# Optimization experiments

Measured on AMD Instinct MI355X. Metric: run time of the kernel, lower is better.

Reference implementation:

```python
import jax, jax.numpy as jnp
import numpy as np

B, S, CACHE, HID, NH, NKV, HD, INTER = 2, 1024, 2048, 2048, 8, 1, 256, 16384
EPS = 1e-6
SOFTCAP = 50.0
SCALE = HD ** -0.5  # query_pre_attn_scalar is None -> head_dim**-0.5
NEG = -1e9


def _rms(x, w, eps=EPS):
    # Gemma RMSNorm: fp32 norm, output scaled by (1 + weight)
    x32 = x.astype(jnp.float32)
    n = x32 * jax.lax.rsqrt(jnp.mean(x32 * x32, axis=-1, keepdims=True) + eps)
    return (n * (1.0 + w)).astype(x.dtype)


def _rope(x, cos, sin):
    # half-split complex rotation (Gemma apply_rotary_emb): first half real, second half imag
    d2 = x.shape[-1] // 2
    x1, x2 = x[..., :d2], x[..., d2:]
    c = cos[None, :, None, :]
    s = sin[None, :, None, :]
    return jnp.concatenate([x1 * c - x2 * s, x1 * s + x2 * c], axis=-1).astype(x.dtype)


def setup_inputs() -> dict:
    key = jax.random.key(0)
    ks = jax.random.split(key, 8)
    sc = lambda k, sh, f: jax.random.normal(k, sh, jnp.float32) * f
    inp = {}
    inp["hidden_states"] = sc(ks[0], (B, S, HID), 1.0)
    inv = 1.0 / (10000.0 ** (np.arange(0, HD, 2, dtype=np.float32) / HD))
    t = np.arange(S, dtype=np.float32)[:, None] * inv[None, :]
    inp["cos"] = jnp.asarray(np.cos(t), jnp.float32)
    inp["sin"] = jnp.asarray(np.sin(t), jnp.float32)
    inp["kv_write_indices"] = jnp.arange(S, dtype=jnp.int32)
    inp["k_cache"] = jnp.zeros((B, CACHE, NKV, HD), jnp.float32)
    inp["v_cache"] = jnp.zeros((B, CACHE, NKV, HD), jnp.float32)
    i = jnp.arange(S)[:, None]
    j = jnp.arange(CACHE)[None, :]
    inp["mask"] = jnp.where(j <= i, 0.0, NEG).astype(jnp.float32)[None, None]  # [1,1,S,CACHE]
    inp["w_qkv"] = sc(ks[1], ((NH + 2 * NKV) * HD, HID), 0.02)
    inp["w_o"] = sc(ks[2], (HID, NH * HD), 0.02)
    inp["w_gate"] = sc(ks[3], (INTER, HID), 0.02)
    inp["w_up"] = sc(ks[4], (INTER, HID), 0.02)
    inp["w_down"] = sc(ks[5], (HID, INTER), 0.02)
    inp["ln_in"] = jnp.zeros((HID,), jnp.float32)
    inp["ln_post"] = jnp.zeros((HID,), jnp.float32)
    inp["q_norm"] = jnp.zeros((HD,), jnp.float32)
    inp["k_norm"] = jnp.zeros((HD,), jnp.float32)
    return inp


def reference(hidden_states, cos, sin, kv_write_indices, k_cache, v_cache, mask,
              w_qkv, w_o, w_gate, w_up, w_down, ln_in, ln_post, q_norm, k_norm):
    # ---- attention sub-block ----
    res = hidden_states
    x = _rms(hidden_states, ln_in)
    qkv = x @ w_qkv.T  # [B,S,(NH+2*NKV)*HD]
    xq, xk, xv = jnp.split(qkv, [NH * HD, NH * HD + NKV * HD], axis=-1)
    xq = xq.reshape(B, S, NH, HD)
    xk = xk.reshape(B, S, NKV, HD)
    xv = xv.reshape(B, S, NKV, HD)
    xq = _rms(xq, q_norm)  # QK-norm
    xk = _rms(xk, k_norm)
    xq = _rope(xq, cos, sin)
    xk = _rope(xk, cos, sin)
    # KV-cache write (index_copy_ on dim 1)
    k_cache = k_cache.at[:, kv_write_indices].set(xk)
    v_cache = v_cache.at[:, kv_write_indices].set(xv)
    key = jnp.repeat(k_cache, NH // NKV, axis=2)  # [B,CACHE,NH,HD]
    val = jnp.repeat(v_cache, NH // NKV, axis=2)
    scores = jnp.einsum('bshd,bthd->bhst', xq * SCALE, key)  # [B,NH,S,CACHE]
    scores = jnp.tanh(scores / SOFTCAP) * SOFTCAP            # logit softcapping
    probs = jax.nn.softmax(scores + mask, axis=-1)
    out = jnp.einsum('bhst,bthd->bshd', probs, val).reshape(B, S, NH * HD)
    h = res + out @ w_o.T
    # ---- MLP sub-block ----
    res = h
    x = _rms(h, ln_post)
    gate = jax.nn.gelu(x @ w_gate.T, approximate=True)
    up = x @ w_up.T
    return res + (gate * up) @ w_down.T
```

## Files before the change

### kernel.cpp

```cpp
#include <hip/hip_runtime.h>
#include <hip/hip_bf16.h>

typedef __attribute__((ext_vector_type(8))) short short8;
typedef __attribute__((ext_vector_type(4))) float f32x4;
typedef unsigned short u16;

#define B_N 2
#define S_N 1024
#define HID_N 2048
#define NH_N 8
#define HD_N 256
#define INTER_N 16384

#define GLB(p) ((const __attribute__((address_space(1))) void*)(p))
#define AS3(p) ((__attribute__((address_space(3))) void*)(p))

__device__ inline u16 f2b_rn(float f) {
    union { float f; unsigned int u; } x; x.f = f;
    unsigned int r = x.u + 0x7fffu + ((x.u >> 16) & 1u);
    return (u16)(r >> 16);
}
__device__ inline float b2f(u16 h) {
    union { unsigned int u; float f; } x; x.u = ((unsigned int)h) << 16;
    return x.f;
}
__device__ inline float gelu_tanh(float x) {
    float x3 = x * x * x;
    return 0.5f * x * (1.f + tanhf(0.7978845608028654f * (x + 0.044715f * x3)));
}

__global__ __launch_bounds__(256) void convert_f2b(const float* __restrict__ in,
                                                   u16* __restrict__ out, int n4) {
    int i = blockIdx.x * 256 + threadIdx.x;
    int stride = gridDim.x * 256;
    for (; i < n4; i += stride) {
        float4 v = reinterpret_cast<const float4*>(in)[i];
        u16 o[4] = { f2b_rn(v.x), f2b_rn(v.y), f2b_rn(v.z), f2b_rn(v.w) };
        reinterpret_cast<ulonglong1*>(out)[i] = *reinterpret_cast<ulonglong1*>(o);
    }
}

__global__ __launch_bounds__(256) void rmsnorm_k(const float* __restrict__ x,
                                                 const float* __restrict__ w,
                                                 u16* __restrict__ out) {
    const int row = blockIdx.x;
    const int tid = threadIdx.x;
    const float* xr = x + (size_t)row * HID_N;
    const float4* xr4 = reinterpret_cast<const float4*>(xr);
    float4 a = xr4[tid * 2], b = xr4[tid * 2 + 1];
    float s = a.x*a.x + a.y*a.y + a.z*a.z + a.w*a.w
            + b.x*b.x + b.y*b.y + b.z*b.z + b.w*b.w;
    for (int off = 32; off > 0; off >>= 1) s += __shfl_xor(s, off, 64);
    __shared__ float red[4];
    if ((tid & 63) == 0) red[tid >> 6] = s;
    __syncthreads();
    float tot = red[0] + red[1] + red[2] + red[3];
    float inv = rsqrtf(tot * (1.0f / HID_N) + 1e-6f);
    const float4* w4 = reinterpret_cast<const float4*>(w);
    float4 wa = w4[tid * 2], wb = w4[tid * 2 + 1];
    short8 o;
    o[0] = (short)f2b_rn(a.x * inv * (1.f + wa.x));
    o[1] = (short)f2b_rn(a.y * inv * (1.f + wa.y));
    o[2] = (short)f2b_rn(a.z * inv * (1.f + wa.z));
    o[3] = (short)f2b_rn(a.w * inv * (1.f + wa.w));
    o[4] = (short)f2b_rn(b.x * inv * (1.f + wb.x));
    o[5] = (short)f2b_rn(b.y * inv * (1.f + wb.y));
    o[6] = (short)f2b_rn(b.z * inv * (1.f + wb.z));
    o[7] = (short)f2b_rn(b.w * inv * (1.f + wb.w));
    reinterpret_cast<short8*>(out + (size_t)row * HID_N)[tid] = o;
}

__global__ __launch_bounds__(256) void qkv_post_k(const float* __restrict__ qkv,
                                                  const float* __restrict__ cosb,
                                                  const float* __restrict__ sinb,
                                                  const int* __restrict__ kvw,
                                                  const float* __restrict__ qn,
                                                  const float* __restrict__ kn,
                                                  u16* __restrict__ qb,
                                                  u16* __restrict__ kb,
                                                  u16* __restrict__ vt) {
    const int bs = blockIdx.x;
    const int b = bs >> 10, s = bs & 1023;
    const int tid = threadIdx.x;
    const float* row = qkv + (size_t)bs * 2560;
    __shared__ float buf[256];
    __shared__ float red[4];
    const int sdst = kvw[s];
    const float cv = cosb[s * 128 + (tid & 127)];
    const float sv = sinb[s * 128 + (tid & 127)];
    for (int vi = 0; vi < 9; ++vi) {
        float val = row[vi * 256 + tid];
        float ss = val * val;
        for (int off = 32; off > 0; off >>= 1) ss += __shfl_xor(ss, off, 64);
        __syncthreads();
        if ((tid & 63) == 0) red[tid >> 6] = ss;
        __syncthreads();
        float ms = (red[0] + red[1] + red[2] + red[3]) * (1.f / 256.f) + 1e-6f;
        const float* nw = (vi < 8) ? qn : kn;
        float nrm = val * rsqrtf(ms) * (1.f + nw[tid]);
        buf[tid] = nrm;
        __syncthreads();
        float o;
        if (tid < 128) o = buf[tid] * cv - buf[tid + 128] * sv;
        else           o = buf[tid - 128] * sv + buf[tid] * cv;
        if (vi < 8) {
            qb[(((size_t)(b * 8 + vi)) * 1024 + s) * 256 + tid] = f2b_rn(o * 0.0625f);
        } else {
            kb[((size_t)(b * 1024 + sdst)) * 256 + tid] = f2b_rn(o);
        }
    }
    float vv = row[2304 + tid];
    vt[((size_t)(b * 256 + tid)) * 1024 + sdst] = f2b_rn(vv);
}

__global__ __launch_bounds__(256) void attn_k(const u16* __restrict__ qb,
                                              const u16* __restrict__ kb,
                                              const u16* __restrict__ vt,
                                              u16* __restrict__ out) {
    const int qt = blockIdx.x;
    const int h  = blockIdx.y;
    const int b  = blockIdx.z;
    const int tid = threadIdx.x, lane = tid & 63, wid = tid >> 6;
    const int g = lane >> 4, li = lane & 15;
    const int q0 = qt * 64 + wid * 16;
    __shared__ u16 pbuf[4][16 * 32];

    short8 qf[8];
    const size_t qbase = (((size_t)(b * 8 + h)) * 1024 + q0 + li) * 256;
    #pragma unroll
    for (int kk = 0; kk < 8; ++kk)
        qf[kk] = *reinterpret_cast<const short8*>(qb + qbase + kk * 32 + g * 8);

    f32x4 o[16];
    #pragma unroll
    for (int d = 0; d < 16; ++d) o[d] = f32x4{0.f, 0.f, 0.f, 0.f};
    float lsum[4] = {0.f, 0.f, 0.f, 0.f};

    const int nt = (qt * 64 + 64) / 32;
    for (int t = 0; t < nt; ++t) {
        const int kv0 = t * 32;
        f32x4 sc[2];
        sc[0] = f32x4{0.f, 0.f, 0.f, 0.f};
        sc[1] = f32x4{0.f, 0.f, 0.f, 0.f};
        #pragma unroll
        for (int ch = 0; ch < 2; ++ch) {
            const size_t kbase = ((size_t)(b * 1024 + kv0 + ch * 16 + li)) * 256;
            #pragma unroll
            for (int kk = 0; kk < 8; ++kk) {
                short8 kf = *reinterpret_cast<const short8*>(kb + kbase + kk * 32 + g * 8);
                sc[ch] = __builtin_amdgcn_mfma_f32_16x16x32_bf16(qf[kk], kf, sc[ch], 0, 0, 0);
            }
        }
        float pv[2][4];
        #pragma unroll
        for (int reg = 0; reg < 4; ++reg) {
            int qrow = q0 + g * 4 + reg;
            float rs = 0.f;
            #pragma unroll
            for (int ch = 0; ch < 2; ++ch) {
                int col = kv0 + ch * 16 + li;
                float s = sc[ch][reg];
                s = tanhf(s * 0.02f) * 50.f;
                float p = (col <= qrow) ? exp2f(s * 1.44269504f) : 0.f;
                pv[ch][reg] = p;
                rs += p;
            }
            for (int off = 1; off < 16; off <<= 1) rs += __shfl_xor(rs, off, 64);
            lsum[reg] += rs;
        }
        __syncthreads();
        #pragma unroll
        for (int reg = 0; reg < 4; ++reg)
            #pragma unroll
            for (int ch = 0; ch < 2; ++ch)
                pbuf[wid][(g * 4 + reg) * 32 + ch * 16 + li] = f2b_rn(pv[ch][reg]);
        __syncthreads();
        short8 pf = *reinterpret_cast<const short8*>(&pbuf[wid][li * 32 + g * 8]);
        #pragma unroll
        for (int dt = 0; dt < 16; ++dt) {
            const size_t vbase = ((size_t)(b * 256 + dt * 16 + li)) * 1024 + kv0 + g * 8;
            short8 vf = *reinterpret_cast<const short8*>(vt + vbase);
            o[dt] = __builtin_amdgcn_mfma_f32_16x16x32_bf16(pf, vf, o[dt], 0, 0, 0);
        }
    }
    #pragma unroll
    for (int reg = 0; reg < 4; ++reg) {
        int row = q0 + g * 4 + reg;
        float inv = 1.f / lsum[reg];
        #pragma unroll
        for (int dt = 0; dt < 16; ++dt) {
            out[((size_t)(b * 1024 + row)) * 2048 + h * 256 + dt * 16 + li] =
                f2b_rn(o[dt][reg] * inv);
        }
    }
}

template <int EPI>
__global__ __launch_bounds__(256) void gemm_bt(const u16* __restrict__ A,
                                               const u16* __restrict__ W,
                                               const float* __restrict__ res,
                                               float* __restrict__ outf,
                                               int M, int N, int K) {
    __shared__ u16 As[2][128 * 64];
    __shared__ u16 Bs[2][128 * 64];
    const int tid = threadIdx.x, lane = tid & 63, wid = tid >> 6;
    const int g = lane >> 4, li = lane & 15;
    const int wr = wid >> 1, wc = wid & 1;
    const int m0 = blockIdx.x * 128, n0 = blockIdx.y * 128;

    f32x4 acc[4][4];
    #pragma unroll
    for (int m = 0; m < 4; ++m)
        #pragma unroll
        for (int n = 0; n < 4; ++n) acc[m][n] = f32x4{0.f, 0.f, 0.f, 0.f};

    const int lrow = lane >> 3;
    const int lcol = (lane & 7) ^ lrow;
    const u16* ga0 = A + (size_t)(m0 + wid * 32 + lrow) * K + lcol * 8;
    const u16* gb0 = W + (size_t)(n0 + wid * 32 + lrow) * K + lcol * 8;
    const int lbase = wid * 32 * 64;

    auto STAGE = [&](int buf, int k0) {
        #pragma unroll
        for (int i = 0; i < 4; ++i) {
            __builtin_amdgcn_global_load_lds(GLB(ga0 + k0 + (size_t)(i * 8) * K),
                                             AS3(&As[buf][lbase + i * 8 * 64]), 16, 0, 0);
            __builtin_amdgcn_global_load_lds(GLB(gb0 + k0 + (size_t)(i * 8) * K),
                                             AS3(&Bs[buf][lbase + i * 8 * 64]), 16, 0, 0);
        }
    };

    const int NT = K >> 6;
    STAGE(0, 0);
    int cur = 0;
    for (int t = 0; t < NT; ++t) {
        if (t + 1 < NT) {
            STAGE(cur ^ 1, (t + 1) << 6);
            asm volatile("s_waitcnt vmcnt(8)" ::: "memory");
        } else {
            asm volatile("s_waitcnt vmcnt(0)" ::: "memory");
        }
        __builtin_amdgcn_s_barrier();
        __builtin_amdgcn_sched_barrier(0);
        #pragma unroll
        for (int kh = 0; kh < 2; ++kh) {
            short8 af[4], bfr[4];
            #pragma unroll
            for (int m = 0; m < 4; ++m) {
                int rw = wr * 64 + m * 16 + li;
                int slot = (kh * 4 + g) ^ (rw & 7);
                af[m] = *reinterpret_cast<const short8*>(&As[cur][rw * 64 + slot * 8]);
            }
            #pragma unroll
            for (int n = 0; n < 4; ++n) {
                int rw = wc * 64 + n * 16 + li;
                int slot = (kh * 4 + g) ^ (rw & 7);
                bfr[n] = *reinterpret_cast<const short8*>(&Bs[cur][rw * 64 + slot * 8]);
            }
            #pragma unroll
            for (int m = 0; m < 4; ++m)
                #pragma unroll
                for (int n = 0; n < 4; ++n)
                    acc[m][n] = __builtin_amdgcn_mfma_f32_16x16x32_bf16(af[m], bfr[n], acc[m][n], 0, 0, 0);
        }
        __builtin_amdgcn_sched_barrier(0);
        __builtin_amdgcn_s_barrier();
        cur ^= 1;
    }

    #pragma unroll
    for (int m = 0; m < 4; ++m) {
        #pragma unroll
        for (int n = 0; n < 4; ++n) {
            #pragma unroll
            for (int reg = 0; reg < 4; ++reg) {
                int row = m0 + wr * 64 + m * 16 + g * 4 + reg;
                int col = n0 + wc * 64 + n * 16 + li;
                size_t idx = (size_t)row * N + col;
                float v = acc[m][n][reg];
                if (EPI == 0) outf[idx] = v;
                else          outf[idx] = v + res[idx];
            }
        }
    }
}

template <int EPI>
__global__ __launch_bounds__(512, 2) void gemm256(const u16* __restrict__ A,
                                                  const u16* __restrict__ W,
                                                  const u16* __restrict__ gin,
                                                  float* __restrict__ outf,
                                                  u16* __restrict__ outb,
                                                  int M, int N, int K, int kcN) {
    __shared__ u16 As_[2][256 * 64];
    __shared__ u16 Bs_[2][256 * 64];
    const int tid = threadIdx.x, lane = tid & 63, wid = tid >> 6;
    const int g = lane >> 4, li = lane & 15;
    const int wm = wid >> 2, wn = wid & 3;
    const int m0 = blockIdx.x * 256, n0 = blockIdx.y * 256;

    int koff = 0, Keff = K;
    if (EPI == 4) {
        Keff = K / kcN;
        koff = blockIdx.z * Keff;
        outf += (size_t)blockIdx.z * M * N;
    }

    f32x4 acc[8][4];
    #pragma unroll
    for (int m = 0; m < 8; ++m)
        #pragma unroll
        for (int n = 0; n < 4; ++n) acc[m][n] = f32x4{0.f, 0.f, 0.f, 0.f};

    const int trow = tid >> 3;
    const int sgr = (tid & 7) ^ (trow & 7);
    const u16* gaS = A + (size_t)(m0 + trow) * K + koff + sgr * 8;
    const u16* gbS = W + (size_t)(n0 + trow) * K + koff + sgr * 8;
    const int ldst = (wid << 9);

    auto STAGE = [&](int buf, int k0) {
        #pragma unroll
        for (int i = 0; i < 4; ++i)
            __builtin_amdgcn_global_load_lds(GLB(gaS + k0 + (size_t)(i * 64) * K),
                                             AS3(&As_[buf][(i << 12) + ldst]), 16, 0, 0);
        #pragma unroll
        for (int i = 0; i < 4; ++i)
            __builtin_amdgcn_global_load_lds(GLB(gbS + k0 + (size_t)(i * 64) * K),
                                             AS3(&Bs_[buf][(i << 12) + ldst]), 16, 0, 0);
    };

    const int NT = Keff >> 6;
    STAGE(0, 0);
    int cur = 0;
    for (int t = 0; t < NT; ++t) {
        if (t + 1 < NT) {
            STAGE(cur ^ 1, (t + 1) << 6);
            asm volatile("s_waitcnt vmcnt(8)" ::: "memory");
        } else {
            asm volatile("s_waitcnt vmcnt(0)" ::: "memory");
        }
        __builtin_amdgcn_s_barrier();
        __builtin_amdgcn_sched_barrier(0);
        #pragma unroll
        for (int kh = 0; kh < 2; ++kh) {
            short8 af[8], bfr[4];
            #pragma unroll
            for (int m = 0; m < 8; ++m) {
                int rw = wm * 128 + m * 16 + li;
                int slot = (kh * 4 + g) ^ (rw & 7);
                af[m] = *reinterpret_cast<const short8*>(&As_[cur][rw * 64 + slot * 8]);
            }
            #pragma unroll
            for (int n = 0; n < 4; ++n) {
                int rw = wn * 64 + n * 16 + li;
                int slot = (kh * 4 + g) ^ (rw & 7);
                bfr[n] = *reinterpret_cast<const short8*>(&Bs_[cur][rw * 64 + slot * 8]);
            }
            #pragma unroll
            for (int m = 0; m < 8; ++m)
                #pragma unroll
                for (int n = 0; n < 4; ++n)
                    acc[m][n] = __builtin_amdgcn_mfma_f32_16x16x32_bf16(af[m], bfr[n], acc[m][n], 0, 0, 0);
        }
        __builtin_amdgcn_sched_barrier(0);
        __builtin_amdgcn_s_barrier();
        cur ^= 1;
    }

    #pragma unroll
    for (int m = 0; m < 8; ++m) {
        #pragma unroll
        for (int n = 0; n < 4; ++n) {
            #pragma unroll
            for (int reg = 0; reg < 4; ++reg) {
                int row = m0 + wm * 128 + m * 16 + g * 4 + reg;
                int col = n0 + wn * 64 + n * 16 + li;
                size_t idx = (size_t)row * N + col;
                float v = acc[m][n][reg];
                if (EPI == 2)      outb[idx] = f2b_rn(gelu_tanh(v));
                else if (EPI == 3) outb[idx] = f2b_rn(v * b2f(gin[idx]));
                else               outf[idx] = v;
            }
        }
    }
}

__global__ __launch_bounds__(256) void reduce4_k(const float* __restrict__ part,
                                                 const float* __restrict__ res,
                                                 float* __restrict__ out, int n4) {
    int i = blockIdx.x * 256 + threadIdx.x;
    int stride = gridDim.x * 256;
    const size_t ps = (size_t)HID_N * B_N * S_N / 4;
    const float4* p4 = reinterpret_cast<const float4*>(part);
    const float4* r4 = reinterpret_cast<const float4*>(res);
    float4* o4 = reinterpret_cast<float4*>(out);
    for (; i < n4; i += stride) {
        float4 a = p4[i], b = p4[i + ps], c = p4[i + 2 * ps], d = p4[i + 3 * ps];
        float4 r = r4[i];
        float4 o;
        o.x = r.x + a.x + b.x + c.x + d.x;
        o.y = r.y + a.y + b.y + c.y + d.y;
        o.z = r.z + a.z + b.z + c.z + d.z;
        o.w = r.w + a.w + b.w + c.w + d.w;
        o4[i] = o;
    }
}

extern "C" void kernel_launch(void* const* d_in, const int* in_sizes, int n_in,
                              void* d_out, int out_size, void* d_ws, size_t ws_size,
                              hipStream_t stream) {
    (void)in_sizes; (void)n_in; (void)out_size; (void)ws_size;
    const float* hs     = (const float*)d_in[0];
    const float* cosb   = (const float*)d_in[1];
    const float* sinb   = (const float*)d_in[2];
    const int*   kvw    = (const int*)d_in[3];
    const float* wqkv   = (const float*)d_in[7];
    const float* wo     = (const float*)d_in[8];
    const float* wg     = (const float*)d_in[9];
    const float* wu     = (const float*)d_in[10];
    const float* wd     = (const float*)d_in[11];
    const float* ln_in  = (const float*)d_in[12];
    const float* ln_post= (const float*)d_in[13];
    const float* qn     = (const float*)d_in[14];
    const float* kn     = (const float*)d_in[15];
    float* out = (float*)d_out;

    char* p = (char*)d_ws;
    auto alloc = [&](size_t bytes) {
        char* r = p;
        p += (bytes + 255) & ~(size_t)255;
        return r;
    };
    u16* wqkv_b = (u16*)alloc(2560ull * 2048 * 2);
    u16* wo_b   = (u16*)alloc(2048ull * 2048 * 2);
    u16* wg_b   = (u16*)alloc(16384ull * 2048 * 2);
    u16* wu_b   = (u16*)alloc(16384ull * 2048 * 2);
    u16* wd_b   = (u16*)alloc(2048ull * 16384 * 2);
    u16* xn     = (u16*)alloc(2048ull * 2048 * 2);
    float* qkvf = (float*)alloc(2048ull * 2560 * 4);
    u16* qbuf   = (u16*)alloc(2ull * 8 * 1024 * 256 * 2);
    u16* kbuf   = (u16*)alloc(2ull * 1024 * 256 * 2);
    u16* vtbuf  = (u16*)alloc(2ull * 256 * 1024 * 2);
    u16* attn_o = (u16*)alloc(2048ull * 2048 * 2);
    float* hbuf = (float*)alloc(2048ull * 2048 * 4);
    u16* x2     = (u16*)alloc(2048ull * 2048 * 2);
    u16* actb   = (u16*)alloc(2048ull * 16384 * 2);
    float* partials = (float*)d_ws;

    auto conv = [&](const float* src, u16* dst, long n) {
        int n4 = (int)(n / 4);
        long blk = (n4 + 255) / 256;
        if (blk > 4096) blk = 4096;
        convert_f2b<<<dim3((unsigned)blk), dim3(256), 0, stream>>>(src, dst, n4);
    };
    conv(wqkv, wqkv_b, 2560l * 2048);
    conv(wo,   wo_b,   2048l * 2048);
    conv(wg,   wg_b,   16384l * 2048);
    conv(wu,   wu_b,   16384l * 2048);
    conv(wd,   wd_b,   2048l * 16384);

    rmsnorm_k<<<dim3(2048), dim3(256), 0, stream>>>(hs, ln_in, xn);
    gemm_bt<0><<<dim3(16, 20), dim3(256), 0, stream>>>(xn, wqkv_b, nullptr,
                                                       qkvf, 2048, 2560, 2048);
    qkv_post_k<<<dim3(2048), dim3(256), 0, stream>>>(qkvf, cosb, sinb, kvw, qn, kn,
                                                     qbuf, kbuf, vtbuf);
    attn_k<<<dim3(16, 8, 2), dim3(256), 0, stream>>>(qbuf, kbuf, vtbuf, attn_o);
    gemm_bt<1><<<dim3(16, 16), dim3(256), 0, stream>>>(attn_o, wo_b, hs,
                                                       hbuf, 2048, 2048, 2048);
    rmsnorm_k<<<dim3(2048), dim3(256), 0, stream>>>(hbuf, ln_post, x2);
    gemm256<2><<<dim3(8, 64), dim3(512), 0, stream>>>(x2, wg_b, nullptr,
                                                      nullptr, actb, 2048, 16384, 2048, 1);
    gemm256<3><<<dim3(8, 64), dim3(512), 0, stream>>>(x2, wu_b, actb,
                                                      nullptr, actb, 2048, 16384, 2048, 1);
    gemm256<4><<<dim3(8, 8, 4), dim3(512), 0, stream>>>(actb, wd_b, nullptr,
                                                        partials, nullptr, 2048, 2048, 16384, 4);
    reduce4_k<<<dim3(2048), dim3(256), 0, stream>>>(partials, hbuf, out, 1048576);
}
```

Measured before the change: 999.0 us.

## Split attention KV range across two chunks with reduction kernel, cheaper softcap

```diff
diff --git a/kernel.cpp b/kernel.cpp
--- a/kernel.cpp
+++ b/kernel.cpp
@@ -116,13 +116,17 @@
 __global__ __launch_bounds__(256) void attn_k(const u16* __restrict__ qb,
                                               const u16* __restrict__ kb,
                                               const u16* __restrict__ vt,
-                                              u16* __restrict__ out) {
+                                              float* __restrict__ po,
+                                              float* __restrict__ pl) {
     const int qt = blockIdx.x;
     const int h  = blockIdx.y;
-    const int b  = blockIdx.z;
+    const int c  = blockIdx.z >> 1;
+    const int b  = blockIdx.z & 1;
+    if (c == 1 && qt < 8) return;
     const int tid = threadIdx.x, lane = tid & 63, wid = tid >> 6;
     const int g = lane >> 4, li = lane & 15;
     const int q0 = qt * 64 + wid * 16;
+    const int kv_lo = c * 512;
     __shared__ u16 pbuf[4][16 * 32];
 
     short8 qf[8];
@@ -131,14 +135,19 @@
     for (int kk = 0; kk < 8; ++kk)
         qf[kk] = *reinterpret_cast<const short8*>(qb + qbase + kk * 32 + g * 8);
 
-    f32x4 o[16];
+    f32x4 o[16], o1;
     #pragma unroll
     for (int d = 0; d < 16; ++d) o[d] = f32x4{0.f, 0.f, 0.f, 0.f};
-    float lsum[4] = {0.f, 0.f, 0.f, 0.f};
-
-    const int nt = (qt * 64 + 64) / 32;
+    o1 = f32x4{0.f, 0.f, 0.f, 0.f};
+    short8 onesf;
+    #pragma unroll
+    for (int j = 0; j < 8; ++j) onesf[j] = (short)0x3F80;
+
+    const int nt = (min(kv_lo + 512, q0 + 16) - kv_lo + 31) >> 5;
+    const int prd = li * 32 + ((g * 8) ^ (((li >> 2) & 3) * 8));
+
     for (int t = 0; t < nt; ++t) {
-        const int kv0 = t * 32;
+        const int kv0 = kv_lo + t * 32;
         f32x4 sc[2];
         sc[0] = f32x4{0.f, 0.f, 0.f, 0.f};
         sc[1] = f32x4{0.f, 0.f, 0.f, 0.f};
@@ -151,48 +160,73 @@
                 sc[ch] = __builtin_amdgcn_mfma_f32_16x16x32_bf16(qf[kk], kf, sc[ch], 0, 0, 0);
             }
         }
-        float pv[2][4];
         #pragma unroll
         for (int reg = 0; reg < 4; ++reg) {
-            int qrow = q0 + g * 4 + reg;
-            float rs = 0.f;
+            const int qrow = q0 + g * 4 + reg;
+            const int prow = g * 4 + reg;
+            const int pswz = ((prow >> 2) & 3) * 8;
             #pragma unroll
             for (int ch = 0; ch < 2; ++ch) {
-                int col = kv0 + ch * 16 + li;
+                const int col = kv0 + ch * 16 + li;
                 float s = sc[ch][reg];
-                s = tanhf(s * 0.02f) * 50.f;
-                float p = (col <= qrow) ? exp2f(s * 1.44269504f) : 0.f;
-                pv[ch][reg] = p;
-                rs += p;
-            }
-            for (int off = 1; off < 16; off <<= 1) rs += __shfl_xor(rs, off, 64);
-            lsum[reg] += rs;
-        }
-        __syncthreads();
-        #pragma unroll
-        for (int reg = 0; reg < 4; ++reg)
-            #pragma unroll
-            for (int ch = 0; ch < 2; ++ch)
-                pbuf[wid][(g * 4 + reg) * 32 + ch * 16 + li] = f2b_rn(pv[ch][reg]);
-        __syncthreads();
-        short8 pf = *reinterpret_cast<const short8*>(&pbuf[wid][li * 32 + g * 8]);
-        #pragma unroll
-        for (int dt = 0; dt < 16; ++dt) {
-            const size_t vbase = ((size_t)(b * 256 + dt * 16 + li)) * 1024 + kv0 + g * 8;
-            short8 vf = *reinterpret_cast<const short8*>(vt + vbase);
-            o[dt] = __builtin_amdgcn_mfma_f32_16x16x32_bf16(pf, vf, o[dt], 0, 0, 0);
-        }
-    }
+                float e = exp2f(s * 0.05770780163555854f);
+                float th = 1.f - 2.f * __builtin_amdgcn_rcpf(e + 1.f);
+                float pv = exp2f(th * 72.13475204444817f);
+                pv = (col <= qrow) ? pv : 0.f;
+                pbuf[wid][prow * 32 + ((ch * 16 + li) ^ pswz)] = f2b_rn(pv);
+            }
+        }
+        short8 pf = *reinterpret_cast<const short8*>(&pbuf[wid][prd]);
+        o1 = __builtin_amdgcn_mfma_f32_16x16x32_bf16(pf, onesf, o1, 0, 0, 0);
+        #pragma unroll
+        for (int dth = 0; dth < 2; ++dth) {
+            short8 vf[8];
+            #pragma unroll
+            for (int d8 = 0; d8 < 8; ++d8) {
+                const int dt = dth * 8 + d8;
+                vf[d8] = *reinterpret_cast<const short8*>(
+                    vt + ((size_t)(b * 256 + dt * 16 + li)) * 1024 + kv0 + g * 8);
+            }
+            #pragma unroll
+            for (int d8 = 0; d8 < 8; ++d8)
+                o[dth * 8 + d8] = __builtin_amdgcn_mfma_f32_16x16x32_bf16(pf, vf[d8], o[dth * 8 + d8], 0, 0, 0);
+        }
+    }
+    const size_t pbase = ((size_t)((c * 2 + b) * 8 + h)) * 1024;
     #pragma unroll
     for (int reg = 0; reg < 4; ++reg) {
-        int row = q0 + g * 4 + reg;
-        float inv = 1.f / lsum[reg];
-        #pragma unroll
-        for (int dt = 0; dt < 16; ++dt) {
-            out[((size_t)(b * 1024 + row)) * 2048 + h * 256 + dt * 16 + li] =
-                f2b_rn(o[dt][reg] * inv);
-        }
-    }
+        const int row = q0 + g * 4 + reg;
+        #pragma unroll
+        for (int dt = 0; dt < 16; ++dt)
+            po[(pbase + row) * 256 + dt * 16 + li] = o[dt][reg];
+        if (li == 0) pl[pbase + row] = o1[reg];
+    }
+}
+
+__global__ __launch_bounds__(256) void attn_red_k(const float* __restrict__ po,
+                                                  const float* __restrict__ pl,
+                                                  u16* __restrict__ out) {
+    const int gid = blockIdx.x;
+    const int b = gid >> 10, s = gid & 1023;
+    const int tid = threadIdx.x;
+    const int h = tid >> 5, d0 = (tid & 31) * 8;
+    const size_t r0 = ((size_t)(b * 8 + h)) * 1024 + s;
+    const size_t r1 = ((size_t)((2 + b) * 8 + h)) * 1024 + s;
+    float l = pl[r0];
+    float4 a0 = *reinterpret_cast<const float4*>(po + r0 * 256 + d0);
+    float4 a1 = *reinterpret_cast<const float4*>(po + r0 * 256 + d0 + 4);
+    if (s >= 512) {
+        l += pl[r1];
+        float4 b0 = *reinterpret_cast<const float4*>(po + r1 * 256 + d0);
+        float4 b1 = *reinterpret_cast<const float4*>(po + r1 * 256 + d0 + 4);
+        a0.x += b0.x; a0.y += b0.y; a0.z += b0.z; a0.w += b0.w;
+        a1.x += b1.x; a1.y += b1.y; a1.z += b1.z; a1.w += b1.w;
+    }
+    const float inv = 1.f / l;
+    u16 r[8] = { f2b_rn(a0.x * inv), f2b_rn(a0.y * inv), f2b_rn(a0.z * inv), f2b_rn(a0.w * inv),
+                 f2b_rn(a1.x * inv), f2b_rn(a1.y * inv), f2b_rn(a1.z * inv), f2b_rn(a1.w * inv) };
+    *reinterpret_cast<ulonglong2*>(out + ((size_t)gid) * 2048 + h * 256 + d0) =
+        *reinterpret_cast<ulonglong2*>(r);
 }
 
 template <int EPI>
@@ -445,6 +479,8 @@
     float* hbuf = (float*)alloc(2048ull * 2048 * 4);
     u16* x2     = (u16*)alloc(2048ull * 2048 * 2);
     u16* actb   = (u16*)alloc(2048ull * 16384 * 2);
+    float* po   = (float*)alloc(4ull * 8 * 1024 * 256 * 4);
+    float* plse = (float*)alloc(4ull * 8 * 1024 * 4);
     float* partials = (float*)d_ws;
 
     auto conv = [&](const float* src, u16* dst, long n) {
@@ -464,7 +500,8 @@
                                                        qkvf, 2048, 2560, 2048);
     qkv_post_k<<<dim3(2048), dim3(256), 0, stream>>>(qkvf, cosb, sinb, kvw, qn, kn,
                                                      qbuf, kbuf, vtbuf);
-    attn_k<<<dim3(16, 8, 2), dim3(256), 0, stream>>>(qbuf, kbuf, vtbuf, attn_o);
+    attn_k<<<dim3(16, 8, 4), dim3(256), 0, stream>>>(qbuf, kbuf, vtbuf, po, plse);
+    attn_red_k<<<dim3(2048), dim3(256), 0, stream>>>(po, plse, attn_o);
     gemm_bt<1><<<dim3(16, 16), dim3(256), 0, stream>>>(attn_o, wo_b, hs,
                                                        hbuf, 2048, 2048, 2048);
     rmsnorm_k<<<dim3(2048), dim3(256), 0, stream>>>(hbuf, ln_post, x2);
```

Result: faster. 890.5 us (-10.9%).
